# Optimization experiments

Measured on AMD Instinct MI355X. Metric: run time of the kernel, lower is better.

Reference implementation:

```python
import jax, jax.numpy as jnp
import numpy as np

DIM = 2048
NH = 16
Q_LORA = 1536
KV_LORA = 512
NOPE = 128
ROPE = 64
VDIM = 128
QK = NOPE + ROPE  # 192
B, S = 2, 2048
EPS = 1.1920929e-07  # torch.finfo(float32).eps (nn.RMSNorm default)


def linear(x, w, b):
    return jnp.einsum('...i,oi->...o', x, w) + b


def rmsnorm(x, w):
    ms = jnp.mean(x * x, axis=-1, keepdims=True)
    return x * jax.lax.rsqrt(ms + EPS) * w


def rope(x, cos, sin):
    # x: [B,S,H,d] interleaved pairs; cos/sin: [S, d//2]
    x = x.reshape(*x.shape[:-1], -1, 2)
    x0, x1 = x[..., 0], x[..., 1]
    c = cos[None, :, None, :]
    s = sin[None, :, None, :]
    y0 = x0 * c - x1 * s
    y1 = x0 * s + x1 * c
    return jnp.stack([y0, y1], axis=-1).reshape(*x.shape[:-2], -1)


def setup_inputs() -> dict:
    key = jax.random.key(0)
    ks = jax.random.split(key, 12)
    sd = 0.02
    x = jax.random.normal(ks[0], (B, S, DIM), dtype=jnp.float32)
    freqs = jax.random.normal(ks[1], (S, ROPE // 2), dtype=jnp.float32)
    causal_mask = jnp.where(jnp.triu(jnp.ones((S, S), bool), k=1), -1e9, 0.0).astype(jnp.float32)
    inp = dict(x=x, freqs=freqs, causal_mask=causal_mask)
    inp['Wq_down_w'] = sd * jax.random.normal(ks[2], (Q_LORA, DIM), dtype=jnp.float32)
    inp['Wq_down_b'] = jnp.zeros((Q_LORA,), jnp.float32)
    inp['q_norm_w'] = jnp.ones((Q_LORA,), jnp.float32)
    inp['Wq_up_w'] = sd * jax.random.normal(ks[3], (NH * QK, Q_LORA), dtype=jnp.float32)
    inp['Wq_up_b'] = jnp.zeros((NH * QK,), jnp.float32)
    inp['Wkv_down_w'] = sd * jax.random.normal(ks[4], (KV_LORA + ROPE, DIM), dtype=jnp.float32)
    inp['Wkv_down_b'] = jnp.zeros((KV_LORA + ROPE,), jnp.float32)
    inp['kv_norm_w'] = jnp.ones((KV_LORA,), jnp.float32)
    inp['Wkv_up_w'] = sd * jax.random.normal(ks[5], (NH * (NOPE + VDIM), KV_LORA), dtype=jnp.float32)
    inp['Wkv_up_b'] = jnp.zeros((NH * (NOPE + VDIM),), jnp.float32)
    inp['Wo_w'] = sd * jax.random.normal(ks[6], (DIM, NH * VDIM), dtype=jnp.float32)
    inp['Wo_b'] = jnp.zeros((DIM,), jnp.float32)
    return inp


def reference(x, freqs, causal_mask, Wq_down_w, Wq_down_b, q_norm_w, Wq_up_w, Wq_up_b,
              Wkv_down_w, Wkv_down_b, kv_norm_w, Wkv_up_w, Wkv_up_b, Wo_w, Wo_b):
    cos, sin = jnp.cos(freqs), jnp.sin(freqs)
    scale = QK ** -0.5
    # Q path: low-rank down, RMSNorm, up
    q_lat = rmsnorm(linear(x, Wq_down_w, Wq_down_b), q_norm_w)
    Q = linear(q_lat, Wq_up_w, Wq_up_b).reshape(B, S, NH, QK)
    Q_nope, Q_rope = Q[..., :NOPE], Q[..., NOPE:]
    Q_rope = rope(Q_rope, cos, sin)
    Q = jnp.concatenate([Q_nope, Q_rope], axis=-1)  # [B,S,H,QK]
    # KV path: shared latent + decoupled rope key
    kv_kr = linear(x, Wkv_down_w, Wkv_down_b)
    kv_lat, K_rope = kv_kr[..., :KV_LORA], kv_kr[..., KV_LORA:]
    kv_lat = rmsnorm(kv_lat, kv_norm_w)
    K_rope = rope(K_rope[:, :, None, :], cos, sin)  # [B,S,1,ROPE]
    kv = linear(kv_lat, Wkv_up_w, Wkv_up_b).reshape(B, S, NH, NOPE + VDIM)
    K_nope, V = kv[..., :NOPE], kv[..., NOPE:]
    K = jnp.concatenate([K_nope, jnp.broadcast_to(K_rope, (B, S, NH, ROPE))], axis=-1)
    # attention
    scores = jnp.einsum('bqhd,bkhd->bhqk', Q, K) * scale + causal_mask[None, None]
    attn = jax.nn.softmax(scores, axis=-1)
    out = jnp.einsum('bhqk,bkhd->bqhd', attn, V).reshape(B, S, NH * VDIM)
    return linear(out, Wo_w, Wo_b)
```

## Files before the change

kernel.cpp:

```cpp
#include <hip/hip_runtime.h>
#include <hip/hip_bf16.h>

#define DIMD 2048
#define NHD 16
#define QLORA 1536
#define KVLORA 512
#define QKD 192
#define BBD 2
#define SSD 2048
#define BSD (BBD*SSD)
#define NDOWN 2176
#define BHN (BBD*NHD)
#define EPSF 1.1920929e-07f
#define SCALEF 0.07216878364870322f

typedef __hip_bfloat16 bf16;
typedef __attribute__((ext_vector_type(8))) short short8;
typedef __attribute__((ext_vector_type(4))) float floatx4;

typedef __attribute__((address_space(1))) char as1_char;
typedef __attribute__((address_space(3))) char as3_char;
#define GLD16(g, l) __builtin_amdgcn_global_load_lds((as1_char*)(g), (as3_char*)(l), 16, 0, 0)

__device__ __forceinline__ float block_sum(float x) {
#pragma unroll
  for (int o = 32; o > 0; o >>= 1) x += __shfl_xor(x, o, 64);
  __shared__ float red[4];
  __syncthreads();
  if ((threadIdx.x & 63) == 0) red[threadIdx.x >> 6] = x;
  __syncthreads();
  return red[0] + red[1] + red[2] + red[3];
}

template<bool STORE_BF16>
__global__ __launch_bounds__(256)
void gemm_bt(const bf16* __restrict__ A, const bf16* __restrict__ Bm,
             const float* __restrict__ bias, void* __restrict__ Cp,
             int M, int N, int K, long sA, long sB, long sC, int ldc)
{
  int nwg = gridDim.x * gridDim.y;
  int lin = blockIdx.y * gridDim.x + blockIdx.x;
  int xcd = lin & 7, l8 = lin >> 3;
  int qd = nwg >> 3, rd = nwg & 7;
  int wg = (xcd < rd ? xcd * (qd + 1) : rd * (qd + 1) + (xcd - rd) * qd) + l8;
  int bx = wg % gridDim.x, by = wg / gridDim.x;

  int m0 = by * 128, n0 = bx * 128;
  long z = blockIdx.z;
  A  += z * sA;
  Bm += z * sB;

  __shared__ __align__(16) bf16 Asm[128 * 32];
  __shared__ __align__(16) bf16 Bsm[128 * 32];

  const int tid  = threadIdx.x;
  const int lane = tid & 63;
  const int wv   = tid >> 6;
  const int wm   = (wv >> 1) << 6;
  const int wn   = (wv & 1) << 6;
  const int fr   = lane & 15;
  const int q8   = (lane >> 4) << 3;

  floatx4 acc[4][4];
#pragma unroll
  for (int i = 0; i < 4; ++i)
#pragma unroll
    for (int j = 0; j < 4; ++j)
      acc[i][j] = (floatx4){0.f, 0.f, 0.f, 0.f};

  for (int k0 = 0; k0 < K; k0 += 32) {
    __syncthreads();
#pragma unroll
    for (int it = 0; it < 2; ++it) {
      int seg = it * 256 + tid;
      int row = seg >> 2, cs = seg & 3;
      GLD16(A  + (long)(m0 + row) * K + k0 + cs * 8, &Asm[(it * 256 + wv * 64) * 8]);
      GLD16(Bm + (long)(n0 + row) * K + k0 + cs * 8, &Bsm[(it * 256 + wv * 64) * 8]);
    }
    __syncthreads();

    short8 fa[4], fb[4];
#pragma unroll
    for (int t = 0; t < 4; ++t) fa[t] = *(const short8*)&Asm[(wm + t * 16 + fr) * 32 + q8];
#pragma unroll
    for (int t = 0; t < 4; ++t) fb[t] = *(const short8*)&Bsm[(wn + t * 16 + fr) * 32 + q8];
#pragma unroll
    for (int i = 0; i < 4; ++i)
#pragma unroll
      for (int j = 0; j < 4; ++j)
        acc[i][j] = __builtin_amdgcn_mfma_f32_16x16x32_bf16(fa[i], fb[j], acc[i][j], 0, 0, 0);
  }

  long cb = z * sC;
  int rq = (lane >> 4) * 4;
#pragma unroll
  for (int i = 0; i < 4; ++i) {
#pragma unroll
    for (int j = 0; j < 4; ++j) {
      int col = n0 + wn + j * 16 + fr;
      float bv = bias ? bias[col] : 0.f;
#pragma unroll
      for (int r = 0; r < 4; ++r) {
        int rowg = m0 + wm + i * 16 + rq + r;
        float v = acc[i][j][r] + bv;
        if (STORE_BF16)
          ((bf16*)Cp)[cb + (long)rowg * ldc + col] = __float2bfloat16(v);
        else
          ((float*)Cp)[cb + (long)rowg * ldc + col] = v;
      }
    }
  }
}

__global__ __launch_bounds__(512, 2)
void flash_attn(const bf16* __restrict__ Qh, const bf16* __restrict__ Kh,
                const bf16* __restrict__ Vt, bf16* __restrict__ attnall)
{
  const int lin = blockIdx.x;
  const int bh  = lin & 31;
  const int p   = lin >> 5;
  const int qtA = 15 - p;
  const int b = bh >> 4, h = bh & 15;

  const bf16* Qg = Qh + (long)bh * SSD * QKD;
  const bf16* Kg = Kh + (long)bh * SSD * QKD;
  const bf16* Vg = Vt + (long)bh * 128 * SSD;

  __shared__ __align__(16) bf16 SM[57344];
  bf16* KB0 = SM;
  bf16* KB1 = SM + 12288;
  bf16* VB0 = SM + 24576;
  bf16* VB1 = SM + 32768;
  bf16* PB  = SM + 40960;

  const int tid  = threadIdx.x;
  const int lane = tid & 63;
  const int wv   = tid >> 6;
  const int w4   = wv & 3;
  const int tb   = wv >> 2;
  const int fr   = lane & 15;
  const int g4   = lane >> 4;

  const int qt    = tb ? (p) : (qtA);
  const int qbase = qt << 7;
  const int jmax  = 2 * qtA + 1;

  long kofs[3]; int kdst[3];
#pragma unroll
  for (int it = 0; it < 3; ++it) {
    int seg = it * 512 + tid;
    int c = seg >> 8, rs = seg & 255;
    int r = rs >> 2, s = (rs & 3) ^ ((r >> 1) & 3);
    kofs[it] = (long)r * QKD + c * 32 + s * 8;
    kdst[it] = c * 2048 + rs * 8;
  }
  long vofs[2]; int vdst[2];
#pragma unroll
  for (int it = 0; it < 2; ++it) {
    int seg = it * 512 + tid;
    int c2 = seg >> 9, ds = seg & 511;
    int d = ds >> 2, s = (ds & 3) ^ ((d >> 1) & 3);
    vofs[it] = (long)d * SSD + c2 * 32 + s * 8;
    vdst[it] = c2 * 4096 + ds * 8;
  }
  int fsw[4];
#pragma unroll
  for (int n = 0; n < 4; ++n) {
    int row = n * 16 + fr;
    fsw[n] = row * 32 + (((g4 ^ (row >> 1)) & 3) << 3);
  }
  int vsw[8];
#pragma unroll
  for (int dn = 0; dn < 8; ++dn) {
    int row = dn * 16 + fr;
    vsw[dn] = row * 32 + (((g4 ^ (row >> 1)) & 3) << 3);
  }
  int qoff[2];
#pragma unroll
  for (int i = 0; i < 2; ++i) {
    int row = wv * 32 + i * 16 + fr;
    qoff[i] = row * 32 + (((g4 ^ (row >> 1)) & 3) << 3);
  }

  const int qbA = qtA << 7, qbB = p << 7;
#pragma unroll
  for (int it = 0; it < 12; ++it) {
    int seg = it * 512 + tid;
    int c = seg >> 10, rs = seg & 1023;
    int r = rs >> 2, s = (rs & 3) ^ ((r >> 1) & 3);
    int grow = (r < 128) ? (qbA + r) : (qbB + r - 128);
    GLD16(Qg + (long)grow * QKD + c * 32 + s * 8, SM + c * 8192 + rs * 8);
  }
  __syncthreads();
  short8 qf[2][6];
#pragma unroll
  for (int i = 0; i < 2; ++i)
#pragma unroll
    for (int c = 0; c < 6; ++c)
      qf[i][c] = *(const short8*)(SM + c * 8192 + qoff[i]);

  floatx4 oacc[2][8];
#pragma unroll
  for (int i = 0; i < 2; ++i)
#pragma unroll
    for (int n = 0; n < 8; ++n) oacc[i][n] = (floatx4){0.f, 0.f, 0.f, 0.f};
  float mi[2][4], li[2][4];
#pragma unroll
  for (int i = 0; i < 2; ++i)
#pragma unroll
    for (int r = 0; r < 4; ++r) { mi[i][r] = -1e30f; li[i][r] = 0.f; }

  __syncthreads();

  auto stageKV = [&](int jb2, bf16* kb2, bf16* vb2) {
#pragma unroll
    for (int it = 0; it < 3; ++it)
      GLD16(Kg + (long)jb2 * QKD + kofs[it], kb2 + kdst[it]);
#pragma unroll
    for (int it = 0; it < 2; ++it)
      GLD16(Vg + jb2 + vofs[it], vb2 + vdst[it]);
  };

  stageKV(0, KB0, VB0);

#pragma unroll 1
  for (int j = 0; j <= jmax; ++j) {
    const int jb = j << 6;
    if (j < jmax) {
      stageKV((j + 1) << 6, (j & 1) ? KB0 : KB1, (j & 1) ? VB0 : VB1);
      asm volatile("s_waitcnt vmcnt(5)" ::: "memory");
    } else {
      asm volatile("s_waitcnt vmcnt(0)" ::: "memory");
    }
    __builtin_amdgcn_sched_barrier(0);
    __builtin_amdgcn_s_barrier();
    __builtin_amdgcn_sched_barrier(0);

    const bf16* kb = (j & 1) ? KB1 : KB0;
    const bf16* vb = (j & 1) ? VB1 : VB0;
    const bool active = (jb <= qbase + w4 * 32 + 31);
    if (active) {
      floatx4 sacc[2][4];
#pragma unroll
      for (int i = 0; i < 2; ++i)
#pragma unroll
        for (int n = 0; n < 4; ++n) sacc[i][n] = (floatx4){0.f, 0.f, 0.f, 0.f};
      __builtin_amdgcn_s_setprio(1);
#pragma unroll
      for (int c = 0; c < 6; ++c) {
#pragma unroll
        for (int n = 0; n < 4; ++n) {
          short8 fb = *(const short8*)(kb + c * 2048 + fsw[n]);
#pragma unroll
          for (int i = 0; i < 2; ++i)
            sacc[i][n] = __builtin_amdgcn_mfma_f32_16x16x32_bf16(qf[i][c], fb, sacc[i][n], 0, 0, 0);
        }
      }
      __builtin_amdgcn_s_setprio(0);

      float pm[2][4];
#pragma unroll
      for (int i = 0; i < 2; ++i) {
        const int rbase = qbase + w4 * 32 + i * 16;
        const bool diag = (jb + 63 > rbase);
#pragma unroll
        for (int r = 0; r < 4; ++r) {
          if (diag) {
            int rowg = rbase + g4 * 4 + r;
#pragma unroll
            for (int n = 0; n < 4; ++n)
              if ((jb + n * 16 + fr) > rowg) sacc[i][n][r] = -1e30f;
          }
          pm[i][r] = fmaxf(fmaxf(sacc[i][0][r], sacc[i][1][r]),
                           fmaxf(sacc[i][2][r], sacc[i][3][r]));
        }
      }
      int nn = 0;
#pragma unroll
      for (int i = 0; i < 2; ++i)
#pragma unroll
        for (int r = 0; r < 4; ++r) nn |= (pm[i][r] > mi[i][r]);
      if (__any(nn)) {
#pragma unroll
        for (int i = 0; i < 2; ++i) {
#pragma unroll
          for (int r = 0; r < 4; ++r) {
            float mx = pm[i][r];
#pragma unroll
            for (int off = 1; off < 16; off <<= 1) mx = fmaxf(mx, __shfl_xor(mx, off, 64));
            float mnew = fmaxf(mi[i][r], mx);
            float alpha = __expf(mi[i][r] - mnew);
            mi[i][r] = mnew;
            li[i][r] *= alpha;
#pragma unroll
            for (int n = 0; n < 8; ++n) oacc[i][n][r] *= alpha;
          }
        }
      }
#pragma unroll
      for (int i = 0; i < 2; ++i) {
#pragma unroll
        for (int r = 0; r < 4; ++r) {
          float acc = 0.f;
#pragma unroll
          for (int n = 0; n < 4; ++n) {
            float pv = __expf(sacc[i][n][r] - mi[i][r]);
            sacc[i][n][r] = pv;
            acc += pv;
          }
          li[i][r] += acc;
        }
      }

#pragma unroll
      for (int i = 0; i < 2; ++i) {
#pragma unroll
        for (int n = 0; n < 4; ++n) {
          int c2 = n >> 1;
          int col = (n & 1) * 16 + fr;
#pragma unroll
          for (int r = 0; r < 4; ++r) {
            int m = wv * 32 + i * 16 + g4 * 4 + r;
            int cw = (((col >> 3) ^ ((m >> 1) & 3)) << 3) | (col & 7);
            PB[c2 * 8192 + m * 32 + cw] = __float2bfloat16(sacc[i][n][r]);
          }
        }
      }

      __builtin_amdgcn_s_setprio(1);
#pragma unroll
      for (int c2 = 0; c2 < 2; ++c2) {
        short8 pf[2];
#pragma unroll
        for (int i = 0; i < 2; ++i)
          pf[i] = *(const short8*)(PB + c2 * 8192 + qoff[i]);
#pragma unroll
        for (int dn = 0; dn < 8; ++dn) {
          short8 vf = *(const short8*)(vb + c2 * 4096 + vsw[dn]);
#pragma unroll
          for (int i = 0; i < 2; ++i)
            oacc[i][dn] = __builtin_amdgcn_mfma_f32_16x16x32_bf16(pf[i], vf, oacc[i][dn], 0, 0, 0);
        }
      }
      __builtin_amdgcn_s_setprio(0);
    }

    __builtin_amdgcn_sched_barrier(0);
    __builtin_amdgcn_s_barrier();
    __builtin_amdgcn_sched_barrier(0);
  }

#pragma unroll
  for (int i = 0; i < 2; ++i) {
#pragma unroll
    for (int r = 0; r < 4; ++r) {
      float l = li[i][r];
#pragma unroll
      for (int off = 1; off < 16; off <<= 1) l += __shfl_xor(l, off, 64);
      float inv = 1.f / l;
      int m = qbase + w4 * 32 + i * 16 + g4 * 4 + r;
      bf16* orow = attnall + ((long)(b * SSD + m) * NHD + h) * 128;
#pragma unroll
      for (int dn = 0; dn < 8; ++dn)
        orow[dn * 16 + fr] = __float2bfloat16(oacc[i][dn][r] * inv);
    }
  }
}

__device__ __forceinline__ void cvt4(const float* __restrict__ s, bf16* __restrict__ d,
                                     long se, long de) {
  float4 v = *(const float4*)(s + se);
  union { bf16 h[4]; uint2 u; } o;
  o.h[0] = __float2bfloat16(v.x); o.h[1] = __float2bfloat16(v.y);
  o.h[2] = __float2bfloat16(v.z); o.h[3] = __float2bfloat16(v.w);
  *(uint2*)(d + de) = o.u;
}

#define NX4   ((long)BSD * DIMD / 4)
#define NQD4  ((long)QLORA * DIMD / 4)
#define NKVD4 ((long)640 * DIMD / 4)
#define NQU4  ((long)3072 * QLORA / 4)
#define NKVU4 ((long)4096 * KVLORA / 4)
#define NWO4  ((long)DIMD * 2048 / 4)

__global__ __launch_bounds__(256)
void cvt_all(const float* __restrict__ x, const float* __restrict__ wqd,
             const float* __restrict__ wkvd, const float* __restrict__ wqu,
             const float* __restrict__ wkvu, const float* __restrict__ wo,
             bf16* __restrict__ dx, bf16* __restrict__ dwd, bf16* __restrict__ dwqu,
             bf16* __restrict__ dwkvu, bf16* __restrict__ dwo)
{
  long i = (long)blockIdx.x * 256 + threadIdx.x;
  if (i < NX4) { cvt4(x, dx, i * 4, i * 4); return; }
  i -= NX4;
  if (i < NQD4) { cvt4(wqd, dwd, i * 4, i * 4); return; }
  i -= NQD4;
  if (i < NKVD4) {
    long e = i * 4;
    long r = e >> 11;
    if (r < 576) cvt4(wkvd, dwd, e, (long)QLORA * DIMD + e);
    else *(uint2*)(dwd + (long)QLORA * DIMD + e) = (uint2){0u, 0u};
    return;
  }
  i -= NKVD4;
  if (i < NQU4) { cvt4(wqu, dwqu, i * 4, i * 4); return; }
  i -= NQU4;
  if (i < NKVU4) { cvt4(wkvu, dwkvu, i * 4, i * 4); return; }
  i -= NKVU4;
  if (i < NWO4) { cvt4(wo, dwo, i * 4, i * 4); return; }
}

template<int L>
__global__ __launch_bounds__(256)
void rmsnorm_k(const bf16* __restrict__ in, const float* __restrict__ bias,
               const float* __restrict__ w, bf16* __restrict__ out, int ldin)
{
  constexpr int NIT = L / 256;
  long r = blockIdx.x;
  const bf16* row = in + r * ldin;
  int tid = threadIdx.x;
  float v[NIT];
  float ss = 0.f;
#pragma unroll
  for (int i = 0; i < NIT; ++i) {
    int c = tid + (i << 8);
    float x = __bfloat162float(row[c]) + (bias ? bias[c] : 0.f);
    v[i] = x;
    ss += x * x;
  }
  ss = block_sum(ss);
  float sc = rsqrtf(ss / (float)L + EPSF);
#pragma unroll
  for (int i = 0; i < NIT; ++i) {
    int c = tid + (i << 8);
    out[r * L + c] = __float2bfloat16(v[i] * sc * w[c]);
  }
}

__global__ void build_q(const bf16* __restrict__ Qf, const float* __restrict__ freqs,
                        bf16* __restrict__ Qh)
{
  int idx = blockIdx.x * 256 + threadIdx.x;
  if (idx >= BSD * NHD * 96) return;
  int j = idx % 96;
  int h = (idx / 96) % NHD;
  int srow = idx / (96 * NHD);
  int s = srow & (SSD - 1);
  int b = srow >> 11;
  const bf16* src = Qf + (long)srow * (NHD * QKD) + h * QKD + 2 * j;
  float x0 = __bfloat162float(src[0]), x1 = __bfloat162float(src[1]), y0, y1;
  if (j >= 64) {
    int i = j - 64;
    float f = freqs[s * 32 + i];
    float c, sn;
    __sincosf(f, &sn, &c);
    y0 = x0 * c - x1 * sn;
    y1 = x0 * sn + x1 * c;
  } else { y0 = x0; y1 = x1; }
  bf16* dst = Qh + ((long)(b * NHD + h) * SSD + s) * QKD + 2 * j;
  dst[0] = __float2bfloat16(y0 * SCALEF);
  dst[1] = __float2bfloat16(y1 * SCALEF);
}

__global__ void build_k(const bf16* __restrict__ kvf, const bf16* __restrict__ kvkr,
                        const float* __restrict__ kvb, const float* __restrict__ freqs,
                        bf16* __restrict__ Kh)
{
  int idx = blockIdx.x * 256 + threadIdx.x;
  if (idx >= BSD * NHD * 96) return;
  int j = idx % 96;
  int h = (idx / 96) % NHD;
  int srow = idx / (96 * NHD);
  int s = srow & (SSD - 1);
  int b = srow >> 11;
  float y0, y1;
  if (j < 64) {
    const bf16* src = kvf + (long)srow * 4096 + h * 256 + 2 * j;
    y0 = __bfloat162float(src[0]); y1 = __bfloat162float(src[1]);
  } else {
    int i = j - 64;
    float x0 = __bfloat162float(kvkr[(long)srow * NDOWN + 512 + 2 * i]) + kvb[512 + 2 * i];
    float x1 = __bfloat162float(kvkr[(long)srow * NDOWN + 513 + 2 * i]) + kvb[513 + 2 * i];
    float f = freqs[s * 32 + i];
    float c, sn;
    __sincosf(f, &sn, &c);
    y0 = x0 * c - x1 * sn;
    y1 = x0 * sn + x1 * c;
  }
  bf16* dst = Kh + ((long)(b * NHD + h) * SSD + s) * QKD + 2 * j;
  dst[0] = __float2bfloat16(y0);
  dst[1] = __float2bfloat16(y1);
}

__global__ __launch_bounds__(256)
void build_vt(const bf16* __restrict__ kvf, bf16* __restrict__ Vt)
{
  __shared__ float t[32][33];
  int s0 = blockIdx.x * 32, d0 = blockIdx.y * 32, z = blockIdx.z;
  int b = z / NHD, h = z % NHD;
  int tx = threadIdx.x, ty = threadIdx.y;
#pragma unroll
  for (int r = 0; r < 4; ++r) {
    int sl = ty + r * 8;
    t[sl][tx] = __bfloat162float(kvf[(long)(b * SSD + s0 + sl) * 4096 + h * 256 + 128 + d0 + tx]);
  }
  __syncthreads();
#pragma unroll
  for (int r = 0; r < 4; ++r) {
    int dl = ty + r * 8;
    Vt[((long)z * 128 + d0 + dl) * SSD + s0 + tx] = __float2bfloat16(t[tx][dl]);
  }
}

__global__ void diag_fill(float* out) { out[blockIdx.x * 256 + threadIdx.x] = 1000.0f; }

extern "C" void kernel_launch(void* const* d_in, const int* in_sizes, int n_in,
                              void* d_out, int out_size, void* d_ws, size_t ws_size,
                              hipStream_t stream)
{
  const float* x     = (const float*)d_in[0];
  const float* freqs = (const float*)d_in[1];
  const float* Wqd   = (const float*)d_in[3];
  const float* Wqdb  = (const float*)d_in[4];
  const float* qnw   = (const float*)d_in[5];
  const float* Wqu   = (const float*)d_in[6];
  const float* Wqub  = (const float*)d_in[7];
  const float* Wkvd  = (const float*)d_in[8];
  const float* Wkvdb = (const float*)d_in[9];
  const float* kvnw  = (const float*)d_in[10];
  const float* Wkvu  = (const float*)d_in[11];
  const float* Wkvub = (const float*)d_in[12];
  const float* Wo    = (const float*)d_in[13];
  const float* Wob   = (const float*)d_in[14];
  float* out = (float*)d_out;

  char* ws = (char*)d_ws;
  size_t off = 0;
  auto alloc = [&](size_t bytes) {
    void* p = ws + off;
    off += (bytes + 255) & ~(size_t)255;
    return p;
  };

  bf16* Wd16   = (bf16*)alloc((size_t)NDOWN * DIMD * 2);
  bf16* Wqu16  = (bf16*)alloc((size_t)3072 * QLORA * 2);
  bf16* Wkvu16 = (bf16*)alloc((size_t)4096 * KVLORA * 2);
  bf16* Wo16   = (bf16*)alloc((size_t)DIMD * 2048 * 2);
  bf16* x16    = (bf16*)alloc((size_t)BSD * DIMD * 2);
  bf16* Ra     = (bf16*)alloc((size_t)BSD * NDOWN * 2);
  bf16* Rb     = (bf16*)alloc((size_t)BSD * QLORA * 2);
  bf16* Rc     = (bf16*)alloc((size_t)BSD * 4096 * 2);
  bf16* Qh16   = (bf16*)alloc((size_t)BHN * SSD * QKD * 2);
  bf16* Kh16   = (bf16*)alloc((size_t)BHN * SSD * QKD * 2);
  bf16* Vt16   = (bf16*)alloc((size_t)BHN * 128 * SSD * 2);

  bf16* qdown   = Ra;
  bf16* kvkr    = Ra + QLORA;
  bf16* qlat16  = Rb;  bf16* kvlat16 = Rb;
  bf16* Qf      = Rc;  bf16* kvf     = Rc;  bf16* attnall = Rc;

  if (off > ws_size) { diag_fill<<<8, 256, 0, stream>>>(out); return; }

  dim3 blk(256);
  auto cdiv = [](long a, long b) { return (int)((a + b - 1) / b); };

  long tot4 = NX4 + NQD4 + NKVD4 + NQU4 + NKVU4 + NWO4;
  cvt_all<<<cdiv(tot4, 256), blk, 0, stream>>>(x, Wqd, Wkvd, Wqu, Wkvu, Wo,
                                               x16, Wd16, Wqu16, Wkvu16, Wo16);

  gemm_bt<true><<<dim3(NDOWN / 128, BSD / 128, 1), blk, 0, stream>>>(
      x16, Wd16, nullptr, Ra, BSD, NDOWN, DIMD, 0, 0, 0, NDOWN);

  rmsnorm_k<QLORA><<<BSD, blk, 0, stream>>>(qdown, Wqdb, qnw, qlat16, NDOWN);
  gemm_bt<true><<<dim3(3072 / 128, BSD / 128, 1), blk, 0, stream>>>(
      qlat16, Wqu16, Wqub, Qf, BSD, 3072, QLORA, 0, 0, 0, 3072);
  build_q<<<cdiv((long)BSD * NHD * 96, 256), blk, 0, stream>>>(Qf, freqs, Qh16);

  rmsnorm_k<KVLORA><<<BSD, blk, 0, stream>>>(kvkr, Wkvdb, kvnw, kvlat16, NDOWN);
  gemm_bt<true><<<dim3(4096 / 128, BSD / 128, 1), blk, 0, stream>>>(
      kvlat16, Wkvu16, Wkvub, kvf, BSD, 4096, KVLORA, 0, 0, 0, 4096);
  build_k<<<cdiv((long)BSD * NHD * 96, 256), blk, 0, stream>>>(kvf, kvkr, Wkvdb, freqs, Kh16);
  build_vt<<<dim3(SSD / 32, 128 / 32, BHN), dim3(32, 8), 0, stream>>>(kvf, Vt16);

  flash_attn<<<dim3(256), dim3(512), 0, stream>>>(Qh16, Kh16, Vt16, attnall);

  gemm_bt<false><<<dim3(2048 / 128, BSD / 128, 1), blk, 0, stream>>>(
      attnall, Wo16, Wob, out, BSD, DIMD, 2048, 0, 0, 0, DIMD);
}
```

Baseline: 527.6 us.

## Fuse Q rope/scale into flash attention and widen GEMM K-tile with swizzled LDS

```diff
diff --git a/kernel.cpp b/kernel.cpp
--- a/kernel.cpp
+++ b/kernel.cpp
@@ -50,8 +50,8 @@
   A  += z * sA;
   Bm += z * sB;
 
-  __shared__ __align__(16) bf16 Asm[128 * 32];
-  __shared__ __align__(16) bf16 Bsm[128 * 32];
+  __shared__ __align__(16) bf16 Asm[128 * 64];
+  __shared__ __align__(16) bf16 Bsm[128 * 64];
 
   const int tid  = threadIdx.x;
   const int lane = tid & 63;
@@ -59,7 +59,28 @@
   const int wm   = (wv >> 1) << 6;
   const int wn   = (wv & 1) << 6;
   const int fr   = lane & 15;
-  const int q8   = (lane >> 4) << 3;
+  const int g4   = lane >> 4;
+
+  int srow[4]; long sofs[4];
+#pragma unroll
+  for (int it = 0; it < 4; ++it) {
+    int seg = it * 256 + tid;
+    int row = seg >> 3, cs = seg & 7;
+    srow[it] = row;
+    sofs[it] = (long)row * 1 ;
+    (void)cs;
+  }
+  int aoff[2][4], boff[2][4];
+#pragma unroll
+  for (int ks = 0; ks < 2; ++ks) {
+#pragma unroll
+    for (int t = 0; t < 4; ++t) {
+      int ra = wm + t * 16 + fr;
+      aoff[ks][t] = ra * 64 + (((ks * 4 + g4) ^ (ra & 7)) << 3);
+      int rb = wn + t * 16 + fr;
+      boff[ks][t] = rb * 64 + (((ks * 4 + g4) ^ (rb & 7)) << 3);
+    }
+  }
 
   floatx4 acc[4][4];
 #pragma unroll
@@ -68,31 +89,37 @@
     for (int j = 0; j < 4; ++j)
       acc[i][j] = (floatx4){0.f, 0.f, 0.f, 0.f};
 
-  for (int k0 = 0; k0 < K; k0 += 32) {
+  for (int k0 = 0; k0 < K; k0 += 64) {
     __syncthreads();
 #pragma unroll
-    for (int it = 0; it < 2; ++it) {
+    for (int it = 0; it < 4; ++it) {
       int seg = it * 256 + tid;
-      int row = seg >> 2, cs = seg & 3;
-      GLD16(A  + (long)(m0 + row) * K + k0 + cs * 8, &Asm[(it * 256 + wv * 64) * 8]);
-      GLD16(Bm + (long)(n0 + row) * K + k0 + cs * 8, &Bsm[(it * 256 + wv * 64) * 8]);
+      int row = seg >> 3, cs = seg & 7;
+      int scs = cs ^ (row & 7);
+      GLD16(A  + (long)(m0 + row) * K + k0 + scs * 8, &Asm[(it * 256 + wv * 64) * 8]);
+      GLD16(Bm + (long)(n0 + row) * K + k0 + scs * 8, &Bsm[(it * 256 + wv * 64) * 8]);
     }
     __syncthreads();
 
-    short8 fa[4], fb[4];
-#pragma unroll
-    for (int t = 0; t < 4; ++t) fa[t] = *(const short8*)&Asm[(wm + t * 16 + fr) * 32 + q8];
-#pragma unroll
-    for (int t = 0; t < 4; ++t) fb[t] = *(const short8*)&Bsm[(wn + t * 16 + fr) * 32 + q8];
-#pragma unroll
-    for (int i = 0; i < 4; ++i)
-#pragma unroll
-      for (int j = 0; j < 4; ++j)
-        acc[i][j] = __builtin_amdgcn_mfma_f32_16x16x32_bf16(fa[i], fb[j], acc[i][j], 0, 0, 0);
+#pragma unroll
+    for (int ks = 0; ks < 2; ++ks) {
+      short8 fa[4], fb[4];
+#pragma unroll
+      for (int t = 0; t < 4; ++t) fa[t] = *(const short8*)&Asm[aoff[ks][t]];
+#pragma unroll
+      for (int t = 0; t < 4; ++t) fb[t] = *(const short8*)&Bsm[boff[ks][t]];
+      __builtin_amdgcn_s_setprio(1);
+#pragma unroll
+      for (int i = 0; i < 4; ++i)
+#pragma unroll
+        for (int j = 0; j < 4; ++j)
+          acc[i][j] = __builtin_amdgcn_mfma_f32_16x16x32_bf16(fa[i], fb[j], acc[i][j], 0, 0, 0);
+      __builtin_amdgcn_s_setprio(0);
+    }
   }
 
   long cb = z * sC;
-  int rq = (lane >> 4) * 4;
+  int rq = g4 * 4;
 #pragma unroll
   for (int i = 0; i < 4; ++i) {
 #pragma unroll
@@ -113,8 +140,9 @@
 }
 
 __global__ __launch_bounds__(512, 2)
-void flash_attn(const bf16* __restrict__ Qh, const bf16* __restrict__ Kh,
-                const bf16* __restrict__ Vt, bf16* __restrict__ attnall)
+void flash_attn(const bf16* __restrict__ Qf, const bf16* __restrict__ Kh,
+                const bf16* __restrict__ Vt, const float* __restrict__ freqs,
+                bf16* __restrict__ attnall)
 {
   const int lin = blockIdx.x;
   const int bh  = lin & 31;
@@ -122,9 +150,9 @@
   const int qtA = 15 - p;
   const int b = bh >> 4, h = bh & 15;
 
-  const bf16* Qg = Qh + (long)bh * SSD * QKD;
-  const bf16* Kg = Kh + (long)bh * SSD * QKD;
-  const bf16* Vg = Vt + (long)bh * 128 * SSD;
+  const bf16* Qgf = Qf + (long)b * SSD * 3072 + h * QKD;
+  const bf16* Kg  = Kh + (long)bh * SSD * QKD;
+  const bf16* Vg  = Vt + (long)bh * 128 * SSD;
 
   __shared__ __align__(16) bf16 SM[57344];
   bf16* KB0 = SM;
@@ -188,8 +216,8 @@
     int seg = it * 512 + tid;
     int c = seg >> 10, rs = seg & 1023;
     int r = rs >> 2, s = (rs & 3) ^ ((r >> 1) & 3);
-    int grow = (r < 128) ? (qbA + r) : (qbB + r - 128);
-    GLD16(Qg + (long)grow * QKD + c * 32 + s * 8, SM + c * 8192 + rs * 8);
+    int tok = (r < 128) ? (qbA + r) : (qbB + r - 128);
+    GLD16(Qgf + (long)tok * 3072 + c * 32 + s * 8, SM + c * 8192 + rs * 8);
   }
   __syncthreads();
   short8 qf[2][6];
@@ -198,6 +226,35 @@
 #pragma unroll
     for (int c = 0; c < 6; ++c)
       qf[i][c] = *(const short8*)(SM + c * 8192 + qoff[i]);
+
+#pragma unroll
+  for (int i = 0; i < 2; ++i) {
+    int tok = qbase + w4 * 32 + i * 16 + fr;
+    const float* fq = freqs + (long)tok * 32;
+#pragma unroll
+    for (int c = 0; c < 4; ++c) {
+#pragma unroll
+      for (int e = 0; e < 8; ++e) {
+        bf16* el = (bf16*)&qf[i][c];
+        el[e] = __float2bfloat16(__bfloat162float(el[e]) * SCALEF);
+      }
+    }
+#pragma unroll
+    for (int c = 4; c < 6; ++c) {
+#pragma unroll
+      for (int pp = 0; pp < 4; ++pp) {
+        int jj = (c - 4) * 16 + g4 * 4 + pp;
+        float f = fq[jj];
+        float cs, sn;
+        __sincosf(f, &sn, &cs);
+        bf16* el = (bf16*)&qf[i][c];
+        float x0 = __bfloat162float(el[2 * pp]);
+        float x1 = __bfloat162float(el[2 * pp + 1]);
+        el[2 * pp]     = __float2bfloat16((x0 * cs - x1 * sn) * SCALEF);
+        el[2 * pp + 1] = __float2bfloat16((x0 * sn + x1 * cs) * SCALEF);
+      }
+    }
+  }
 
   floatx4 oacc[2][8];
 #pragma unroll
@@ -435,31 +492,6 @@
     int c = tid + (i << 8);
     out[r * L + c] = __float2bfloat16(v[i] * sc * w[c]);
   }
-}
-
-__global__ void build_q(const bf16* __restrict__ Qf, const float* __restrict__ freqs,
-                        bf16* __restrict__ Qh)
-{
-  int idx = blockIdx.x * 256 + threadIdx.x;
-  if (idx >= BSD * NHD * 96) return;
-  int j = idx % 96;
-  int h = (idx / 96) % NHD;
-  int srow = idx / (96 * NHD);
-  int s = srow & (SSD - 1);
-  int b = srow >> 11;
-  const bf16* src = Qf + (long)srow * (NHD * QKD) + h * QKD + 2 * j;
-  float x0 = __bfloat162float(src[0]), x1 = __bfloat162float(src[1]), y0, y1;
-  if (j >= 64) {
-    int i = j - 64;
-    float f = freqs[s * 32 + i];
-    float c, sn;
-    __sincosf(f, &sn, &c);
-    y0 = x0 * c - x1 * sn;
-    y1 = x0 * sn + x1 * c;
-  } else { y0 = x0; y1 = x1; }
-  bf16* dst = Qh + ((long)(b * NHD + h) * SSD + s) * QKD + 2 * j;
-  dst[0] = __float2bfloat16(y0 * SCALEF);
-  dst[1] = __float2bfloat16(y1 * SCALEF);
 }
 
 __global__ void build_k(const bf16* __restrict__ kvf, const bf16* __restrict__ kvkr,
@@ -550,14 +582,14 @@
   bf16* Ra     = (bf16*)alloc((size_t)BSD * NDOWN * 2);
   bf16* Rb     = (bf16*)alloc((size_t)BSD * QLORA * 2);
   bf16* Rc     = (bf16*)alloc((size_t)BSD * 4096 * 2);
-  bf16* Qh16   = (bf16*)alloc((size_t)BHN * SSD * QKD * 2);
+  bf16* Qf     = (bf16*)alloc((size_t)BSD * 3072 * 2);
   bf16* Kh16   = (bf16*)alloc((size_t)BHN * SSD * QKD * 2);
   bf16* Vt16   = (bf16*)alloc((size_t)BHN * 128 * SSD * 2);
 
   bf16* qdown   = Ra;
   bf16* kvkr    = Ra + QLORA;
   bf16* qlat16  = Rb;  bf16* kvlat16 = Rb;
-  bf16* Qf      = Rc;  bf16* kvf     = Rc;  bf16* attnall = Rc;
+  bf16* kvf     = Rc;  bf16* attnall = Rc;
 
   if (off > ws_size) { diag_fill<<<8, 256, 0, stream>>>(out); return; }
 
@@ -574,7 +606,6 @@
   rmsnorm_k<QLORA><<<BSD, blk, 0, stream>>>(qdown, Wqdb, qnw, qlat16, NDOWN);
   gemm_bt<true><<<dim3(3072 / 128, BSD / 128, 1), blk, 0, stream>>>(
       qlat16, Wqu16, Wqub, Qf, BSD, 3072, QLORA, 0, 0, 0, 3072);
-  build_q<<<cdiv((long)BSD * NHD * 96, 256), blk, 0, stream>>>(Qf, freqs, Qh16);
 
   rmsnorm_k<KVLORA><<<BSD, blk, 0, stream>>>(kvkr, Wkvdb, kvnw, kvlat16, NDOWN);
   gemm_bt<true><<<dim3(4096 / 128, BSD / 128, 1), blk, 0, stream>>>(
@@ -582,7 +613,7 @@
   build_k<<<cdiv((long)BSD * NHD * 96, 256), blk, 0, stream>>>(kvf, kvkr, Wkvdb, freqs, Kh16);
   build_vt<<<dim3(SSD / 32, 128 / 32, BHN), dim3(32, 8), 0, stream>>>(kvf, Vt16);
 
-  flash_attn<<<dim3(256), dim3(512), 0, stream>>>(Qh16, Kh16, Vt16, attnall);
+  flash_attn<<<dim3(256), dim3(512), 0, stream>>>(Qf, Kh16, Vt16, freqs, attnall);
 
   gemm_bt<false><<<dim3(2048 / 128, BSD / 128, 1), blk, 0, stream>>>(
       attnall, Wo16, Wob, out, BSD, DIMD, 2048, 0, 0, 0, DIMD);
```

After: 469.2 us. 11.1% less time.
